# Kernel tuning notes

Measured on AMD Instinct MI355X. Metric: run time of the kernel, lower is better.

The kernel has to match this reference:

```python
import jax, jax.numpy as jnp
import numpy as np

N_NODES = 8192
N_EDGES = 524288
N_PAIRS = 262144
N_TYPES = 86


def _gcn_conv(x, W, b, src, dst, n):
    # PyG GCNConv: transform, add self-loops, symmetric degree normalization,
    # scatter-add aggregation at destination nodes.
    xw = x @ W  # [N, F_out]
    loop = jnp.arange(n, dtype=src.dtype)
    s = jnp.concatenate([src, loop])
    d = jnp.concatenate([dst, loop])
    deg = jax.ops.segment_sum(jnp.ones(d.shape, xw.dtype), d, num_segments=n)
    dinv = jnp.where(deg > 0, jax.lax.rsqrt(deg), 0.0)  # deg^{-1/2}, 0 for isolated
    coef = dinv[s] * dinv[d]  # [E+N]
    out = jax.ops.segment_sum(xw[s] * coef[:, None], d, num_segments=n)
    return out + b


def setup_inputs() -> dict:
    key = jax.random.key(0)
    ks = jax.random.split(key, 10)
    x = jax.random.normal(ks[0], (N_NODES, N_NODES), dtype=jnp.float32)
    edge_index = jax.random.randint(ks[1], (2, N_EDGES), 0, N_NODES, dtype=jnp.int32)
    drug1_idx = jax.random.randint(ks[2], (N_PAIRS,), 0, N_NODES, dtype=jnp.int32)
    drug2_idx = jax.random.randint(ks[3], (N_PAIRS,), 0, N_NODES, dtype=jnp.int32)
    W1 = jax.random.normal(ks[4], (N_NODES, 128), dtype=jnp.float32) / np.sqrt(N_NODES)
    b1 = jnp.zeros((128,), jnp.float32)
    W2 = jax.random.normal(ks[5], (128, 64), dtype=jnp.float32) / np.sqrt(128.0)
    b2 = jnp.zeros((64,), jnp.float32)
    Wfc = jax.random.normal(ks[6], (128, N_TYPES), dtype=jnp.float32) / np.sqrt(128.0)
    bfc = jnp.zeros((N_TYPES,), jnp.float32)
    return {"x": x, "edge_index": edge_index, "drug1_idx": drug1_idx,
            "drug2_idx": drug2_idx, "W1": W1, "b1": b1, "W2": W2, "b2": b2,
            "Wfc": Wfc, "bfc": bfc}


def reference(x, edge_index, drug1_idx, drug2_idx, W1, b1, W2, b2, Wfc, bfc):
    n = x.shape[0]
    src, dst = edge_index[0], edge_index[1]
    h = jax.nn.relu(_gcn_conv(x, W1, b1, src, dst, n))
    # dropout p=0.3 is identity at inference (training=False)
    h = jax.nn.relu(_gcn_conv(h, W2, b2, src, dst, n))
    combined = jnp.concatenate([h[drug1_idx], h[drug2_idx]], axis=1)  # [P, 128]
    return jax.nn.sigmoid(combined @ Wfc + bfc)
```

## Files before the change

kernel.cpp:

```cpp
#include <hip/hip_runtime.h>
#include <math.h>
#include <stdint.h>
#include <stddef.h>

#define N_NODES 8192
#define N_EDGES 524288
#define N_PAIRS 262144
#define N_TYPES 86
#define F1 128
#define F2 64

typedef unsigned short ushort_t;
typedef unsigned int uint_t;
typedef __attribute__((ext_vector_type(8))) short bfrag;
typedef __attribute__((ext_vector_type(4))) float ffrag;

typedef __attribute__((address_space(3))) char lds_char;
typedef __attribute__((address_space(1))) const char g_char;

__device__ __forceinline__ void gload16(const void* g, void* l) {
  __builtin_amdgcn_global_load_lds((const g_char*)g, (lds_char*)l, 16, 0, 0);
}

__device__ inline ushort_t f2bf(float f) {
  uint_t u = __float_as_uint(f);
  uint_t r = u + 0x7fffu + ((u >> 16) & 1u);
  return (ushort_t)(r >> 16);
}
__device__ inline float bf2f(ushort_t h) {
  return __uint_as_float(((uint_t)h) << 16);
}


__global__ void count_deg_k(const int* __restrict__ dst, int* __restrict__ cnt) {
  int e = blockIdx.x * blockDim.x + threadIdx.x;
  if (e < N_EDGES) atomicAdd(&cnt[dst[e]], 1);
}

__global__ void dinv_k(const int* __restrict__ cnt, float* __restrict__ dinv) {
  int i = blockIdx.x * blockDim.x + threadIdx.x;
  if (i < N_NODES) dinv[i] = 1.0f / sqrtf((float)(cnt[i] + 1));
}

__global__ void scan_k(const int* __restrict__ cnt, int* __restrict__ rp,
                       int* __restrict__ fill) {
  __shared__ int s[1024];
  int t = threadIdx.x;
  int v[8];
  int sum = 0;
#pragma unroll
  for (int i = 0; i < 8; i++) { v[i] = cnt[t * 8 + i]; sum += v[i]; }
  s[t] = sum;
  __syncthreads();
  for (int off = 1; off < 1024; off <<= 1) {
    int add = (t >= off) ? s[t - off] : 0;
    __syncthreads();
    s[t] += add;
    __syncthreads();
  }
  int excl = s[t] - sum;
#pragma unroll
  for (int i = 0; i < 8; i++) {
    rp[t * 8 + i] = excl;
    fill[t * 8 + i] = excl;
    excl += v[i];
  }
  if (t == 1023) rp[N_NODES] = excl;
}

__global__ void scatter_k(const int* __restrict__ src, const int* __restrict__ dst,
                          int* fill, int* __restrict__ csr) {
  int e = blockIdx.x * blockDim.x + threadIdx.x;
  if (e < N_EDGES) {
    int d = dst[e];
    int pos = atomicAdd(&fill[d], 1);
    csr[pos] = src[e];
  }
}


__global__ __launch_bounds__(256) void w1split_k(const float* __restrict__ W1,
                                                 ushort_t* __restrict__ W1th,
                                                 ushort_t* __restrict__ W1tl) {
  __shared__ ushort_t lh[32 * 65];
  __shared__ ushort_t ll[32 * 65];
  int tid = threadIdx.x;
  int k0 = blockIdx.x * 64;
  int n0 = blockIdx.y * 32;
#pragma unroll
  for (int i = 0; i < 8; i++) {
    int c = tid + 256 * i;
    int kr = c >> 5, nc = c & 31;
    float v = W1[(size_t)(k0 + kr) * F1 + n0 + nc];
    ushort_t h = f2bf(v);
    ushort_t l = f2bf(v - bf2f(h));
    lh[nc * 65 + kr] = h;
    ll[nc * 65 + kr] = l;
  }
  __syncthreads();
#pragma unroll
  for (int i = 0; i < 2; i++) {
    int c = tid + 256 * i;
    int buf = c >> 8;
    int cc = c & 255;
    int nr = cc >> 3, kc = cc & 7;
    const ushort_t* l = buf ? ll : lh;
    uint4 u;
    u.x = (uint_t)l[nr * 65 + kc * 8 + 0] | ((uint_t)l[nr * 65 + kc * 8 + 1] << 16);
    u.y = (uint_t)l[nr * 65 + kc * 8 + 2] | ((uint_t)l[nr * 65 + kc * 8 + 3] << 16);
    u.z = (uint_t)l[nr * 65 + kc * 8 + 4] | ((uint_t)l[nr * 65 + kc * 8 + 5] << 16);
    u.w = (uint_t)l[nr * 65 + kc * 8 + 6] | ((uint_t)l[nr * 65 + kc * 8 + 7] << 16);
    ushort_t* dst = (buf ? W1tl : W1th) + (size_t)(n0 + nr) * N_NODES + k0 + kc * 8;
    *(uint4*)dst = u;
  }
}


#define BUFSZ 65536
#define OA_H 0
#define OA_L 16384
#define OB_H 32768
#define OB_L 49152

__global__ __launch_bounds__(512) void gemm1_mfma_k(const float* __restrict__ x,
                                                    const ushort_t* __restrict__ W1th,
                                                    const ushort_t* __restrict__ W1tl,
                                                    float* __restrict__ part, int kspan) {
  __shared__ __align__(16) char lds[2 * BUFSZ];
  int tid = threadIdx.x;
  int m_blk = blockIdx.x * 128;
  int kbase = blockIdx.y * kspan;
  int ktiles = kspan >> 6;
  int wave = tid >> 6, lane = tid & 63;
  int wr = wave >> 2, wc = wave & 3;
  int lrow = lane & 15, kgrp = lane >> 4;
  int xr = (lrow & 7) << 4;
  int kb0 = kgrp * 16;

  const ushort_t* bsrc = (wave < 4) ? W1th : W1tl;
  int b_quarter = (wave & 3) * 4096;
  int ob = (wave < 4) ? OB_H : OB_L;
  int brow_g = (wave & 3) * 32 + (lane >> 3);
  int kel = (((lane & 7) ^ ((lane >> 3) & 7)) << 3);

  ffrag acc[4][2];
#pragma unroll
  for (int mi = 0; mi < 4; mi++)
#pragma unroll
    for (int ni = 0; ni < 2; ni++) acc[mi][ni] = (ffrag)(0.0f);

  float4 av[4];

#define LOADA(K0)                                                                    \
  {                                                                                  \
    _Pragma("unroll") for (int i = 0; i < 4; i++) {                                  \
      int c = tid + 512 * i;                                                         \
      int row = c >> 4, c4 = c & 15;                                                 \
      av[i] = *(const float4*)&x[(size_t)(m_blk + row) * N_NODES + (K0) + 4 * c4];   \
    }                                                                                \
  }

#define LOADB(K0, BUFP)                                                              \
  {                                                                                  \
    _Pragma("unroll") for (int i = 0; i < 4; i++) {                                  \
      const ushort_t* gp = bsrc + (size_t)(brow_g + i * 8) * N_NODES + (K0) + kel;   \
      gload16(gp, (BUFP) + ob + b_quarter + i * 1024);                               \
    }                                                                                \
  }

#define STOREA(BUFP)                                                                 \
  {                                                                                  \
    _Pragma("unroll") for (int i = 0; i < 4; i++) {                                  \
      int c = tid + 512 * i;                                                         \
      int row = c >> 4, c4 = c & 15;                                                 \
      float f0 = av[i].x, f1 = av[i].y, f2 = av[i].z, f3 = av[i].w;                  \
      ushort_t h0 = f2bf(f0), h1 = f2bf(f1), h2 = f2bf(f2), h3 = f2bf(f3);           \
      ushort_t l0 = f2bf(f0 - bf2f(h0)), l1 = f2bf(f1 - bf2f(h1));                   \
      ushort_t l2 = f2bf(f2 - bf2f(h2)), l3 = f2bf(f3 - bf2f(h3));                   \
      uint2 hp, lp;                                                                  \
      hp.x = (uint_t)h0 | ((uint_t)h1 << 16); hp.y = (uint_t)h2 | ((uint_t)h3 << 16);\
      lp.x = (uint_t)l0 | ((uint_t)l1 << 16); lp.y = (uint_t)l2 | ((uint_t)l3 << 16);\
      uint_t off = row * 128 + ((c4 * 8) ^ ((row & 7) << 4));                        \
      *(uint2*)((BUFP) + OA_H + off) = hp;                                           \
      *(uint2*)((BUFP) + OA_L + off) = lp;                                           \
    }                                                                                \
  }

#define COMPUTE(BUFP)                                                                \
  {                                                                                  \
    _Pragma("unroll") for (int ks = 0; ks < 2; ++ks) {                               \
      int cb = ks * 64 + kb0;                                                        \
      bfrag bh[2], bl[2];                                                            \
      _Pragma("unroll") for (int ni = 0; ni < 2; ni++) {                             \
        int brow = wc * 32 + ni * 16 + lrow;                                         \
        uint_t boff = brow * 128 + (cb ^ xr);                                        \
        bh[ni] = *(const bfrag*)((BUFP) + OB_H + boff);                              \
        bl[ni] = *(const bfrag*)((BUFP) + OB_L + boff);                              \
      }                                                                              \
      _Pragma("unroll") for (int mi = 0; mi < 4; mi++) {                             \
        int arow = wr * 64 + mi * 16 + lrow;                                         \
        uint_t aoff = arow * 128 + (cb ^ xr);                                        \
        bfrag ah = *(const bfrag*)((BUFP) + OA_H + aoff);                            \
        bfrag al = *(const bfrag*)((BUFP) + OA_L + aoff);                            \
        _Pragma("unroll") for (int ni = 0; ni < 2; ni++) {                           \
          acc[mi][ni] = __builtin_amdgcn_mfma_f32_16x16x32_bf16(ah, bh[ni], acc[mi][ni], 0, 0, 0); \
          acc[mi][ni] = __builtin_amdgcn_mfma_f32_16x16x32_bf16(ah, bl[ni], acc[mi][ni], 0, 0, 0); \
          acc[mi][ni] = __builtin_amdgcn_mfma_f32_16x16x32_bf16(al, bh[ni], acc[mi][ni], 0, 0, 0); \
        }                                                                            \
      }                                                                              \
    }                                                                                \
  }

  LOADA(kbase);
  LOADB(kbase, lds);
  STOREA(lds);
  __syncthreads();

  int cur = 0;
  for (int kt = 0; kt < ktiles - 1; ++kt) {
    char* bufC = lds + cur * BUFSZ;
    char* bufN = lds + (cur ^ 1) * BUFSZ;
    int k0n = kbase + ((kt + 1) << 6);
    LOADA(k0n);
    LOADB(k0n, bufN);
    __builtin_amdgcn_sched_barrier(0);
    COMPUTE(bufC);
    STOREA(bufN);
    __syncthreads();
    cur ^= 1;
  }
  COMPUTE(lds + cur * BUFSZ);

  float* outp = part + (size_t)blockIdx.y * (N_NODES * F1);
#pragma unroll
  for (int mi = 0; mi < 4; mi++) {
#pragma unroll
    for (int ni = 0; ni < 2; ni++) {
      int col = wc * 32 + ni * 16 + lrow;
#pragma unroll
      for (int r = 0; r < 4; r++) {
        int row = m_blk + wr * 64 + mi * 16 + kgrp * 4 + r;
        outp[(size_t)row * F1 + col] = acc[mi][ni][r];
      }
    }
  }
#undef LOADA
#undef LOADB
#undef STOREA
#undef COMPUTE
}

__global__ void reduceS_k(const float* __restrict__ part, float* __restrict__ xw1, int S) {
  int i = blockIdx.x * blockDim.x + threadIdx.x;
  float4 a = ((const float4*)part)[i];
  for (int s = 1; s < S; s++) {
    float4 b = ((const float4*)(part + (size_t)s * N_NODES * F1))[i];
    a.x += b.x; a.y += b.y; a.z += b.z; a.w += b.w;
  }
  ((float4*)xw1)[i] = a;
}


template <int F>
__global__ void agg_k(const float* __restrict__ xw, const int* __restrict__ csr,
                      const int* __restrict__ rp, const float* __restrict__ dinv,
                      const float* __restrict__ bias, float* __restrict__ hout) {
  int node = blockIdx.x;
  int f = threadIdx.x;
  __shared__ int sidx[F];
  __shared__ float sdv[F];
  int beg = rp[node], end = rp[node + 1];
  float acc = 0.f;
  for (int base = beg; base < end; base += F) {
    int n = end - base;
    if (n > F) n = F;
    __syncthreads();
    if (f < n) {
      int s = csr[base + f];
      sidx[f] = s;
      sdv[f] = dinv[s];
    }
    __syncthreads();
    for (int i = 0; i < n; i++) acc += xw[(size_t)sidx[i] * F + f] * sdv[i];
  }
  float dv = dinv[node];
  float v = (acc + xw[(size_t)node * F + f] * dv) * dv + bias[f];
  hout[(size_t)node * F + f] = v > 0.f ? v : 0.f;
}


__global__ __launch_bounds__(256) void gemm2_k(const float* __restrict__ h1,
                                               const float* __restrict__ W2,
                                               float* __restrict__ xw2) {
  __shared__ float W2s[F1 * F2];
  __shared__ float As[16 * F1];
  int tid = threadIdx.x;
  int r0 = blockIdx.x * 16;
#pragma unroll
  for (int j = 0; j < 8; j++)
    ((float4*)W2s)[tid + 256 * j] = ((const float4*)W2)[tid + 256 * j];
#pragma unroll
  for (int j = 0; j < 2; j++)
    ((float4*)As)[tid + 256 * j] = ((const float4*)(h1 + (size_t)r0 * F1))[tid + 256 * j];
  __syncthreads();
  int r = tid >> 4, c4 = tid & 15;
  float4 acc = make_float4(0.f, 0.f, 0.f, 0.f);
#pragma unroll 8
  for (int k = 0; k < F1; k++) {
    float a = As[r * F1 + k];
    float4 bv = *(float4*)&W2s[k * F2 + 4 * c4];
    acc.x += a * bv.x; acc.y += a * bv.y; acc.z += a * bv.z; acc.w += a * bv.w;
  }
  *(float4*)&xw2[(size_t)(r0 + r) * F2 + 4 * c4] = acc;
}


__global__ void pboth_k(const float* __restrict__ h2, const float* __restrict__ Wfc,
                        float* __restrict__ P) {
  __shared__ float hs[64 * 16];
  int tid = threadIdx.x;
  int r0 = blockIdx.x * 16;
  for (int idx = tid; idx < 256; idx += 192) {
    int row = idx >> 4, k4 = idx & 15;
    float4 h = *(const float4*)&h2[(size_t)(r0 + row) * F2 + 4 * k4];
    hs[(4 * k4 + 0) * 16 + row] = h.x;
    hs[(4 * k4 + 1) * 16 + row] = h.y;
    hs[(4 * k4 + 2) * 16 + row] = h.z;
    hs[(4 * k4 + 3) * 16 + row] = h.w;
  }
  __syncthreads();
  if (tid < 172) {
    int half = tid < 86 ? 0 : 1;
    int j = tid - 86 * half;
    const float* wp = Wfc + (size_t)(64 * half) * N_TYPES + j;
    float acc[16];
#pragma unroll
    for (int r = 0; r < 16; r++) acc[r] = 0.f;
    for (int k = 0; k < 64; k++) {
      float w = wp[(size_t)k * N_TYPES];
      const float* hk = &hs[k * 16];
#pragma unroll
      for (int r = 0; r < 16; r++) acc[r] += hk[r] * w;
    }
#pragma unroll
    for (int r = 0; r < 16; r++) P[(size_t)(r0 + r) * 172 + tid] = acc[r];
  }
}


__global__ void final_k(const float* __restrict__ P, const int* __restrict__ d1,
                        const int* __restrict__ d2, const float* __restrict__ bfc,
                        float* __restrict__ out) {
  int gid = blockIdx.x * blockDim.x + threadIdx.x;
  if (gid >= N_PAIRS * 43) return;
  int p = gid / 43;
  int j = gid - p * 43;
  int a = d1[p], b = d2[p];
  float2 v1 = *(const float2*)&P[(size_t)a * 172 + 2 * j];
  float2 v2 = *(const float2*)&P[(size_t)b * 172 + 86 + 2 * j];
  float2 bb = *(const float2*)&bfc[2 * j];
  float z0 = v1.x + v2.x + bb.x;
  float z1 = v1.y + v2.y + bb.y;
  float2 o;
  o.x = 1.0f / (1.0f + expf(-z0));
  o.y = 1.0f / (1.0f + expf(-z1));
  *(float2*)&out[(size_t)p * 86 + 2 * j] = o;
}


extern "C" void kernel_launch(void* const* d_in, const int* in_sizes, int n_in,
                              void* d_out, int out_size, void* d_ws, size_t ws_size,
                              hipStream_t stream) {
  const float* x   = (const float*)d_in[0];
  const int*   ei  = (const int*)d_in[1];
  const int*   d1  = (const int*)d_in[2];
  const int*   d2  = (const int*)d_in[3];
  const float* W1  = (const float*)d_in[4];
  const float* b1  = (const float*)d_in[5];
  const float* W2  = (const float*)d_in[6];
  const float* b2  = (const float*)d_in[7];
  const float* Wfc = (const float*)d_in[8];
  const float* bfc = (const float*)d_in[9];
  float* out = (float*)d_out;

  const int* esrc = ei;
  const int* edst = ei + N_EDGES;

  char* w = (char*)d_ws;
  size_t off = 0;
  auto alloc = [&](size_t bytes) -> char* {
    char* p = w + off;
    off += (bytes + 255) & ~(size_t)255;
    return p;
  };
  int*      cnt  = (int*)alloc((size_t)N_NODES * 4);
  float*    dinv = (float*)alloc((size_t)N_NODES * 4);
  int*      rp   = (int*)alloc((size_t)(N_NODES + 1) * 4);
  int*      fill = (int*)alloc((size_t)N_NODES * 4);
  int*      csr  = (int*)alloc((size_t)N_EDGES * 4);
  ushort_t* W1th = (ushort_t*)alloc((size_t)N_NODES * F1 * 2);
  ushort_t* W1tl = (ushort_t*)alloc((size_t)N_NODES * F1 * 2);
  float*    h1   = (float*)alloc((size_t)N_NODES * F1 * 4);
  float*    xw2  = (float*)alloc((size_t)N_NODES * F2 * 4);
  float*    h2   = (float*)alloc((size_t)N_NODES * F2 * 4);
  float*    P    = (float*)alloc((size_t)N_NODES * 172 * 4);

  size_t partBytes = (size_t)N_NODES * F1 * 4;
  int S = 4;
  while (S > 1 && off + (size_t)S * partBytes > ws_size) S >>= 1;
  float* part = (float*)alloc((size_t)S * partBytes);
  float* xw1 = part;
  if (off > ws_size) return;

  hipMemsetAsync(cnt, 0, (size_t)N_NODES * 4, stream);
  count_deg_k<<<N_EDGES / 256, 256, 0, stream>>>(edst, cnt);
  dinv_k<<<N_NODES / 256, 256, 0, stream>>>(cnt, dinv);
  scan_k<<<1, 1024, 0, stream>>>(cnt, rp, fill);
  scatter_k<<<N_EDGES / 256, 256, 0, stream>>>(esrc, edst, fill, csr);

  w1split_k<<<dim3(N_NODES / 64, F1 / 32), 256, 0, stream>>>(W1, W1th, W1tl);
  gemm1_mfma_k<<<dim3(N_NODES / 128, S), 512, 0, stream>>>(x, W1th, W1tl, part, N_NODES / S);
  if (S > 1)
    reduceS_k<<<(N_NODES * F1 / 4) / 256, 256, 0, stream>>>(part, xw1, S);
  agg_k<F1><<<N_NODES, F1, 0, stream>>>(xw1, csr, rp, dinv, b1, h1);

  gemm2_k<<<N_NODES / 16, 256, 0, stream>>>(h1, W2, xw2);
  agg_k<F2><<<N_NODES, F2, 0, stream>>>(xw2, csr, rp, dinv, b2, h2);

  pboth_k<<<N_NODES / 16, 192, 0, stream>>>(h2, Wfc, P);
  final_k<<<(N_PAIRS * 43) / 256, 256, 0, stream>>>(P, d1, d2, bfc, out);
}
```

Baseline: 267.7 us.

## Retile GEMM1 to 256 threads with BK=32, split-K 8, and vectorize aggregation

GEMM1 now runs 256-thread blocks: each wave computes a 64x64 tile, the K tile drops from 64 to 32, LDS per buffer is halved, and s_setprio is raised around the MFMA compute. The grid is reordered so the split-K slice is the fast dimension, and split-K goes from 4 to 8. The layer-1 aggregation uses 64 threads, each handling two features with float2 loads, and hipMemsetAsync is replaced by a zeroing kernel. The aim is better occupancy and latency hiding in the main GEMM and fewer threads per aggregation block. In exchange, the larger split-K doubles the partial-sum buffer the reduction must read, and the smaller K tile adds a sync per 32 elements of K.

New measurement: 274.4 us. +2.5%, slower.

```diff
diff --git a/kernel.cpp b/kernel.cpp
--- a/kernel.cpp
+++ b/kernel.cpp
@@ -31,6 +31,10 @@
   return __uint_as_float(((uint_t)h) << 16);
 }
 
+
+__global__ void zero_k(int* __restrict__ p) {
+  p[blockIdx.x * 256 + threadIdx.x] = 0;
+}
 
 __global__ void count_deg_k(const int* __restrict__ dst, int* __restrict__ cnt) {
   int e = blockIdx.x * blockDim.x + threadIdx.x;
@@ -116,63 +120,60 @@
 }
 
 
-#define BUFSZ 65536
+#define BUFSZ 32768
 #define OA_H 0
-#define OA_L 16384
-#define OB_H 32768
-#define OB_L 49152
-
-__global__ __launch_bounds__(512) void gemm1_mfma_k(const float* __restrict__ x,
+#define OA_L 8192
+#define OB_H 16384
+#define OB_L 24576
+
+__global__ __launch_bounds__(256) void gemm1_mfma_k(const float* __restrict__ x,
                                                     const ushort_t* __restrict__ W1th,
                                                     const ushort_t* __restrict__ W1tl,
                                                     float* __restrict__ part, int kspan) {
   __shared__ __align__(16) char lds[2 * BUFSZ];
   int tid = threadIdx.x;
-  int m_blk = blockIdx.x * 128;
-  int kbase = blockIdx.y * kspan;
-  int ktiles = kspan >> 6;
+  int m_blk = blockIdx.y * 128;
+  int kbase = blockIdx.x * kspan;
+  int ktiles = kspan >> 5;
   int wave = tid >> 6, lane = tid & 63;
-  int wr = wave >> 2, wc = wave & 3;
+  int wr = wave >> 1, wc = wave & 1;
   int lrow = lane & 15, kgrp = lane >> 4;
-  int xr = (lrow & 7) << 4;
-  int kb0 = kgrp * 16;
-
-  const ushort_t* bsrc = (wave < 4) ? W1th : W1tl;
-  int b_quarter = (wave & 3) * 4096;
-  int ob = (wave < 4) ? OB_H : OB_L;
-  int brow_g = (wave & 3) * 32 + (lane >> 3);
-  int kel = (((lane & 7) ^ ((lane >> 3) & 7)) << 3);
-
-  ffrag acc[4][2];
+
+  int b_rbase = wave * 16 + (lane >> 2);
+  int b_kel = ((lane & 3) ^ ((lane >> 2) & 3)) * 8;
+
+  ffrag acc[4][4];
 #pragma unroll
   for (int mi = 0; mi < 4; mi++)
 #pragma unroll
-    for (int ni = 0; ni < 2; ni++) acc[mi][ni] = (ffrag)(0.0f);
+    for (int ni = 0; ni < 4; ni++) acc[mi][ni] = (ffrag)(0.0f);
 
   float4 av[4];
 
 #define LOADA(K0)                                                                    \
   {                                                                                  \
     _Pragma("unroll") for (int i = 0; i < 4; i++) {                                  \
-      int c = tid + 512 * i;                                                         \
-      int row = c >> 4, c4 = c & 15;                                                 \
+      int c = tid + 256 * i;                                                         \
+      int row = c >> 3, c4 = c & 7;                                                  \
       av[i] = *(const float4*)&x[(size_t)(m_blk + row) * N_NODES + (K0) + 4 * c4];   \
     }                                                                                \
   }
 
 #define LOADB(K0, BUFP)                                                              \
   {                                                                                  \
-    _Pragma("unroll") for (int i = 0; i < 4; i++) {                                  \
-      const ushort_t* gp = bsrc + (size_t)(brow_g + i * 8) * N_NODES + (K0) + kel;   \
-      gload16(gp, (BUFP) + ob + b_quarter + i * 1024);                               \
+    _Pragma("unroll") for (int i = 0; i < 2; i++) {                                  \
+      const ushort_t* gh = W1th + (size_t)(i * 64 + b_rbase) * N_NODES + (K0) + b_kel; \
+      gload16(gh, (BUFP) + OB_H + i * 4096 + wave * 1024);                           \
+      const ushort_t* gl = W1tl + (size_t)(i * 64 + b_rbase) * N_NODES + (K0) + b_kel; \
+      gload16(gl, (BUFP) + OB_L + i * 4096 + wave * 1024);                           \
     }                                                                                \
   }
 
 #define STOREA(BUFP)                                                                 \
   {                                                                                  \
     _Pragma("unroll") for (int i = 0; i < 4; i++) {                                  \
-      int c = tid + 512 * i;                                                         \
-      int row = c >> 4, c4 = c & 15;                                                 \
+      int c = tid + 256 * i;                                                         \
+      int row = c >> 3, c4 = c & 7;                                                  \
       float f0 = av[i].x, f1 = av[i].y, f2 = av[i].z, f3 = av[i].w;                  \
       ushort_t h0 = f2bf(f0), h1 = f2bf(f1), h2 = f2bf(f2), h3 = f2bf(f3);           \
       ushort_t l0 = f2bf(f0 - bf2f(h0)), l1 = f2bf(f1 - bf2f(h1));                   \
@@ -180,7 +181,7 @@
       uint2 hp, lp;                                                                  \
       hp.x = (uint_t)h0 | ((uint_t)h1 << 16); hp.y = (uint_t)h2 | ((uint_t)h3 << 16);\
       lp.x = (uint_t)l0 | ((uint_t)l1 << 16); lp.y = (uint_t)l2 | ((uint_t)l3 << 16);\
-      uint_t off = row * 128 + ((c4 * 8) ^ ((row & 7) << 4));                        \
+      uint_t off = row * 64 + ((c4 * 8) ^ ((row & 3) << 4));                         \
       *(uint2*)((BUFP) + OA_H + off) = hp;                                           \
       *(uint2*)((BUFP) + OA_L + off) = lp;                                           \
     }                                                                                \
@@ -188,25 +189,22 @@
 
 #define COMPUTE(BUFP)                                                                \
   {                                                                                  \
-    _Pragma("unroll") for (int ks = 0; ks < 2; ++ks) {                               \
-      int cb = ks * 64 + kb0;                                                        \
-      bfrag bh[2], bl[2];                                                            \
-      _Pragma("unroll") for (int ni = 0; ni < 2; ni++) {                             \
-        int brow = wc * 32 + ni * 16 + lrow;                                         \
-        uint_t boff = brow * 128 + (cb ^ xr);                                        \
-        bh[ni] = *(const bfrag*)((BUFP) + OB_H + boff);                              \
-        bl[ni] = *(const bfrag*)((BUFP) + OB_L + boff);                              \
-      }                                                                              \
-      _Pragma("unroll") for (int mi = 0; mi < 4; mi++) {                             \
-        int arow = wr * 64 + mi * 16 + lrow;                                         \
-        uint_t aoff = arow * 128 + (cb ^ xr);                                        \
-        bfrag ah = *(const bfrag*)((BUFP) + OA_H + aoff);                            \
-        bfrag al = *(const bfrag*)((BUFP) + OA_L + aoff);                            \
-        _Pragma("unroll") for (int ni = 0; ni < 2; ni++) {                           \
-          acc[mi][ni] = __builtin_amdgcn_mfma_f32_16x16x32_bf16(ah, bh[ni], acc[mi][ni], 0, 0, 0); \
-          acc[mi][ni] = __builtin_amdgcn_mfma_f32_16x16x32_bf16(ah, bl[ni], acc[mi][ni], 0, 0, 0); \
-          acc[mi][ni] = __builtin_amdgcn_mfma_f32_16x16x32_bf16(al, bh[ni], acc[mi][ni], 0, 0, 0); \
-        }                                                                            \
+    bfrag bh[4], bl[4];                                                              \
+    _Pragma("unroll") for (int ni = 0; ni < 4; ni++) {                               \
+      int brow = wc * 64 + ni * 16 + lrow;                                           \
+      uint_t boff = brow * 64 + ((kgrp * 16) ^ ((brow & 3) << 4));                   \
+      bh[ni] = *(const bfrag*)((BUFP) + OB_H + boff);                                \
+      bl[ni] = *(const bfrag*)((BUFP) + OB_L + boff);                                \
+    }                                                                                \
+    _Pragma("unroll") for (int mi = 0; mi < 4; mi++) {                               \
+      int arow = wr * 64 + mi * 16 + lrow;                                           \
+      uint_t aoff = arow * 64 + ((kgrp * 16) ^ ((arow & 3) << 4));                   \
+      bfrag ah = *(const bfrag*)((BUFP) + OA_H + aoff);                              \
+      bfrag al = *(const bfrag*)((BUFP) + OA_L + aoff);                              \
+      _Pragma("unroll") for (int ni = 0; ni < 4; ni++) {                             \
+        acc[mi][ni] = __builtin_amdgcn_mfma_f32_16x16x32_bf16(ah, bh[ni], acc[mi][ni], 0, 0, 0); \
+        acc[mi][ni] = __builtin_amdgcn_mfma_f32_16x16x32_bf16(ah, bl[ni], acc[mi][ni], 0, 0, 0); \
+        acc[mi][ni] = __builtin_amdgcn_mfma_f32_16x16x32_bf16(al, bh[ni], acc[mi][ni], 0, 0, 0); \
       }                                                                              \
     }                                                                                \
   }
@@ -220,23 +218,27 @@
   for (int kt = 0; kt < ktiles - 1; ++kt) {
     char* bufC = lds + cur * BUFSZ;
     char* bufN = lds + (cur ^ 1) * BUFSZ;
-    int k0n = kbase + ((kt + 1) << 6);
+    int k0n = kbase + ((kt + 1) << 5);
     LOADA(k0n);
     LOADB(k0n, bufN);
     __builtin_amdgcn_sched_barrier(0);
+    __builtin_amdgcn_s_setprio(1);
     COMPUTE(bufC);
+    __builtin_amdgcn_s_setprio(0);
     STOREA(bufN);
     __syncthreads();
     cur ^= 1;
   }
+  __builtin_amdgcn_s_setprio(1);
   COMPUTE(lds + cur * BUFSZ);
-
-  float* outp = part + (size_t)blockIdx.y * (N_NODES * F1);
+  __builtin_amdgcn_s_setprio(0);
+
+  float* outp = part + (size_t)blockIdx.x * (N_NODES * F1);
 #pragma unroll
   for (int mi = 0; mi < 4; mi++) {
 #pragma unroll
-    for (int ni = 0; ni < 2; ni++) {
-      int col = wc * 32 + ni * 16 + lrow;
+    for (int ni = 0; ni < 4; ni++) {
+      int col = wc * 64 + ni * 16 + lrow;
 #pragma unroll
       for (int r = 0; r < 4; r++) {
         int row = m_blk + wr * 64 + mi * 16 + kgrp * 4 + r;
@@ -267,13 +269,13 @@
                       const float* __restrict__ bias, float* __restrict__ hout) {
   int node = blockIdx.x;
   int f = threadIdx.x;
-  __shared__ int sidx[F];
-  __shared__ float sdv[F];
+  __shared__ int sidx[64];
+  __shared__ float sdv[64];
   int beg = rp[node], end = rp[node + 1];
-  float acc = 0.f;
-  for (int base = beg; base < end; base += F) {
+  float ax = 0.f, ay = 0.f;
+  for (int base = beg; base < end; base += 64) {
     int n = end - base;
-    if (n > F) n = F;
+    if (n > 64) n = 64;
     __syncthreads();
     if (f < n) {
       int s = csr[base + f];
@@ -281,11 +283,31 @@
       sdv[f] = dinv[s];
     }
     __syncthreads();
-    for (int i = 0; i < n; i++) acc += xw[(size_t)sidx[i] * F + f] * sdv[i];
+    if constexpr (F == 128) {
+      for (int i = 0; i < n; i++) {
+        float dv = sdv[i];
+        float2 v = ((const float2*)&xw[(size_t)sidx[i] * F])[f];
+        ax += v.x * dv;
+        ay += v.y * dv;
+      }
+    } else {
+      for (int i = 0; i < n; i++) ax += xw[(size_t)sidx[i] * F + f] * sdv[i];
+    }
   }
   float dv = dinv[node];
-  float v = (acc + xw[(size_t)node * F + f] * dv) * dv + bias[f];
-  hout[(size_t)node * F + f] = v > 0.f ? v : 0.f;
+  if constexpr (F == 128) {
+    float2 sv = ((const float2*)&xw[(size_t)node * F])[f];
+    float2 bb = ((const float2*)bias)[f];
+    float vx = (ax + sv.x * dv) * dv + bb.x;
+    float vy = (ay + sv.y * dv) * dv + bb.y;
+    float2 o;
+    o.x = vx > 0.f ? vx : 0.f;
+    o.y = vy > 0.f ? vy : 0.f;
+    ((float2*)&hout[(size_t)node * F])[f] = o;
+  } else {
+    float v = (ax + xw[(size_t)node * F + f] * dv) * dv + bias[f];
+    hout[(size_t)node * F + f] = v > 0.f ? v : 0.f;
+  }
 }
 
 
@@ -406,26 +428,26 @@
   float*    P    = (float*)alloc((size_t)N_NODES * 172 * 4);
 
   size_t partBytes = (size_t)N_NODES * F1 * 4;
-  int S = 4;
+  int S = 8;
   while (S > 1 && off + (size_t)S * partBytes > ws_size) S >>= 1;
   float* part = (float*)alloc((size_t)S * partBytes);
   float* xw1 = part;
   if (off > ws_size) return;
 
-  hipMemsetAsync(cnt, 0, (size_t)N_NODES * 4, stream);
+  zero_k<<<N_NODES / 256, 256, 0, stream>>>(cnt);
   count_deg_k<<<N_EDGES / 256, 256, 0, stream>>>(edst, cnt);
   dinv_k<<<N_NODES / 256, 256, 0, stream>>>(cnt, dinv);
   scan_k<<<1, 1024, 0, stream>>>(cnt, rp, fill);
   scatter_k<<<N_EDGES / 256, 256, 0, stream>>>(esrc, edst, fill, csr);
 
   w1split_k<<<dim3(N_NODES / 64, F1 / 32), 256, 0, stream>>>(W1, W1th, W1tl);
-  gemm1_mfma_k<<<dim3(N_NODES / 128, S), 512, 0, stream>>>(x, W1th, W1tl, part, N_NODES / S);
+  gemm1_mfma_k<<<dim3(S, N_NODES / 128), 256, 0, stream>>>(x, W1th, W1tl, part, N_NODES / S);
   if (S > 1)
     reduceS_k<<<(N_NODES * F1 / 4) / 256, 256, 0, stream>>>(part, xw1, S);
-  agg_k<F1><<<N_NODES, F1, 0, stream>>>(xw1, csr, rp, dinv, b1, h1);
+  agg_k<F1><<<N_NODES, 64, 0, stream>>>(xw1, csr, rp, dinv, b1, h1);
 
   gemm2_k<<<N_NODES / 16, 256, 0, stream>>>(h1, W2, xw2);
-  agg_k<F2><<<N_NODES, F2, 0, stream>>>(xw2, csr, rp, dinv, b2, h2);
+  agg_k<F2><<<N_NODES, 64, 0, stream>>>(xw2, csr, rp, dinv, b2, h2);
 
   pboth_k<<<N_NODES / 16, 192, 0, stream>>>(h2, Wfc, P);
   final_k<<<(N_PAIRS * 43) / 256, 256, 0, stream>>>(P, d1, d2, bfc, out);
```
